# Kernel tuning notes

Hardware: AMD Instinct MI355X
Metric: run time of the kernel (lower is better)

The kernel has to match this reference:

```python
import jax, jax.numpy as jnp
import numpy as np

N = 8000      # nodes (spatial spots)
E = 40000     # directed edges (kNN graph, avg degree 5)
DIN = 1024    # input_dim
H = 3         # heads
C = 1024      # hidden_dim per head
NCLS = 460    # n_classes
NCEN = 100    # centroid count (pass-through only)
NEG_SLOPE = 0.2


def setup_inputs() -> dict:
    key = jax.random.key(0)
    ks = jax.random.split(key, 12)
    s_in = 1.0 / np.sqrt(DIN)   # glorot-ish scale for 1024 fan-in
    s_h = 1.0 / np.sqrt(C)
    return {
        'x': jax.random.normal(ks[0], (N, DIN), jnp.float32),
        'edge_index': jax.random.randint(ks[1], (E, 2), 0, N),  # [E,2] (src,dst)
        'Wl': jax.random.normal(ks[2], (DIN, H * C), jnp.float32) * s_in,
        'bl': jnp.zeros((H * C,), jnp.float32),
        'Wr': jax.random.normal(ks[3], (DIN, H * C), jnp.float32) * s_in,
        'br': jnp.zeros((H * C,), jnp.float32),
        'att': jax.random.normal(ks[4], (H, C), jnp.float32) * s_h,
        'bias': jnp.zeros((C,), jnp.float32),
        'Wf': jax.random.normal(ks[5], (C, NCLS), jnp.float32) * s_h,
        'bf': jnp.zeros((NCLS,), jnp.float32),
        'exps': jax.random.uniform(ks[6], (N, NCLS), jnp.float32),
        'exps_c': jax.random.uniform(ks[7], (NCEN, NCLS), jnp.float32),
    }


def reference(x, edge_index, Wl, bl, Wr, br, att, bias, Wf, bf, exps, exps_c):
    n = x.shape[0]
    h_, c_ = att.shape
    # PyG GATv2Conv default add_self_loops=True
    loops = jnp.arange(n)
    src = jnp.concatenate([edge_index[:, 0], loops])
    dst = jnp.concatenate([edge_index[:, 1], loops])
    # lin_l / lin_r projections -> [N,H,C]
    xl = (x @ Wl + bl).reshape(n, h_, c_)
    xr = (x @ Wr + br).reshape(n, h_, c_)
    # GATv2 edge scores: a^T LeakyReLU(x_l[src] + x_r[dst])  -> [Etot,H]
    s = jax.nn.leaky_relu(xl[src] + xr[dst], NEG_SLOPE)
    e = jnp.einsum('ehc,hc->eh', s, att)
    # segment softmax over incoming edges per dst node (PyG softmax: +1e-16)
    m = jax.lax.stop_gradient(jax.ops.segment_max(e, dst, num_segments=n))
    a = jnp.exp(e - m[dst])
    denom = jax.ops.segment_sum(a, dst, num_segments=n)
    alpha = a / (denom[dst] + 1e-16)
    # weighted scatter-add of source messages
    out = jax.ops.segment_sum(alpha[:, :, None] * xl[src], dst, num_segments=n)
    # concat=False -> mean over heads, then conv bias
    out = out.mean(axis=1) + bias
    # fc + row softmax
    h = jax.nn.softmax(out @ Wf + bf, axis=-1)
    return h
```

## Files before the change

### kernel.cpp

```cpp
#include <hip/hip_runtime.h>

#define NNODES 8000
#define MPAD   8192
#define NEDGES 40000
#define ETOT   (NEDGES + NNODES)
#define DIN    1024
#define NH     3
#define CH     1024
#define HC     (NH * CH)
#define NTOT   (2 * HC)
#define NCLS   460
#define NCLS_P 512
#define NEG    0.2f

typedef _Float16 h8 __attribute__((ext_vector_type(8)));
typedef _Float16 h4v __attribute__((ext_vector_type(4)));
typedef float    f4 __attribute__((ext_vector_type(4)));

#define GLOAD16(g, l) \
    __builtin_amdgcn_global_load_lds((const __attribute__((address_space(1))) void*)(g), \
                                     (__attribute__((address_space(3))) void*)(l), 16, 0, 0)

__global__ __launch_bounds__(256)
void fp16_pad_convert(const float* __restrict__ in, _Float16* __restrict__ out,
                      int rows_in, int rows_out, int cols)
{
    size_t i4 = (size_t)blockIdx.x * 256 + threadIdx.x;
    size_t tot = ((size_t)rows_out * cols) >> 2;
    if (i4 >= tot) return;
    size_t e = i4 << 2;
    int row = (int)(e / cols);
    float vx = 0.f, vy = 0.f, vz = 0.f, vw = 0.f;
    if (row < rows_in) {
        float4 v = *(const float4*)(in + e);
        vx = v.x; vy = v.y; vz = v.z; vw = v.w;
    }
    h4v o = { (_Float16)vx, (_Float16)vy, (_Float16)vz, (_Float16)vw };
    *(h4v*)(out + e) = o;
}

__global__ __launch_bounds__(256)
void transpose_to_fp16(const float* __restrict__ W, _Float16* __restrict__ Wt,
                       int K, int Ncols, int rowOff)
{
    __shared__ float tile[32][33];
    int n0 = blockIdx.x * 32, k0 = blockIdx.y * 32;
    int tx = threadIdx.x, ty = threadIdx.y;
    #pragma unroll
    for (int i = 0; i < 4; ++i) {
        int k = k0 + ty + i * 8;
        int n = n0 + tx;
        tile[ty + i * 8][tx] = (n < Ncols) ? W[(size_t)k * Ncols + n] : 0.f;
    }
    __syncthreads();
    #pragma unroll
    for (int i = 0; i < 4; ++i) {
        int n = n0 + ty + i * 8;
        int k = k0 + tx;
        Wt[(size_t)(rowOff + n) * K + k] = (_Float16)tile[tx][ty + i * 8];
    }
}

__global__ __launch_bounds__(256)
void bias_pack(const float* __restrict__ bl, const float* __restrict__ br,
               const float* __restrict__ bf, const float* __restrict__ att,
               float* __restrict__ b1, float* __restrict__ b2, _Float16* __restrict__ atth)
{
    int i = blockIdx.x * 256 + threadIdx.x;
    if (i < HC) { b1[i] = bl[i]; b1[HC + i] = br[i]; atth[i] = (_Float16)att[i]; }
    if (i < NCLS_P) b2[i] = (i < NCLS) ? bf[i] : 0.f;
}

__global__ __launch_bounds__(256)
void csr_count(const int* __restrict__ ei, int* __restrict__ cnt)
{
    int e = blockIdx.x * 256 + threadIdx.x;
    if (e >= ETOT) return;
    int dst = (e < NEDGES) ? ei[2 * e + 1] : (e - NEDGES);
    atomicAdd(&cnt[dst], 1);
}

__global__ __launch_bounds__(1024)
void csr_scan(const int* __restrict__ cnt, int* __restrict__ rofs)
{
    __shared__ int s[1024];
    int t = threadIdx.x;
    int base = t * 8;
    int local[8];
    int sum = 0;
    #pragma unroll
    for (int i = 0; i < 8; ++i) {
        local[i] = sum;
        sum += (base + i < NNODES) ? cnt[base + i] : 0;
    }
    s[t] = sum;
    __syncthreads();
    for (int off = 1; off < 1024; off <<= 1) {
        int v = (t >= off) ? s[t - off] : 0;
        __syncthreads();
        if (t >= off) s[t] += v;
        __syncthreads();
    }
    int pre = (t > 0) ? s[t - 1] : 0;
    #pragma unroll
    for (int i = 0; i < 8; ++i)
        if (base + i < NNODES) rofs[base + i] = pre + local[i];
}

__global__ __launch_bounds__(256)
void csr_fill(const int* __restrict__ ei, const int* __restrict__ rofs,
              int* __restrict__ cursor, int* __restrict__ csr_src)
{
    int e = blockIdx.x * 256 + threadIdx.x;
    if (e >= ETOT) return;
    int src, dst;
    if (e < NEDGES) { src = ei[2 * e]; dst = ei[2 * e + 1]; }
    else            { src = dst = e - NEDGES; }
    int pos = rofs[dst] + atomicAdd(&cursor[dst], 1);
    csr_src[pos] = src;
}

__global__ __launch_bounds__(512, 2)
void gemm256_f16(const _Float16* __restrict__ A, const _Float16* __restrict__ Bt,
                 const float* __restrict__ biasN, _Float16* __restrict__ C16,
                 int N, int K)
{
    __shared__ __align__(16) _Float16 lds[65536];

    int nwg = gridDim.x;
    int orig = blockIdx.x;
    int cpx = nwg >> 3;
    int wg = (orig & 7) * cpx + (orig >> 3);
    int nbx = N >> 8;
    int bm = wg / nbx, bn = wg - bm * nbx;
    int m0 = bm << 8, n0 = bn << 8;

    const int t = threadIdx.x;
    const int lane = t & 63;
    const int w = t >> 6;
    const int wm = w >> 2;
    const int wn = w & 3;

    const int sRow   = lane >> 3;
    const int sColSw = (((lane & 7) ^ sRow) << 3);
    const int seg0   = w << 1;

    const int l15 = lane & 15;

    f4 acc[8][4];
    f4 zero = { 0.f, 0.f, 0.f, 0.f };
    #pragma unroll
    for (int i = 0; i < 8; ++i)
        #pragma unroll
        for (int j = 0; j < 4; ++j) acc[i][j] = zero;

    auto STAGE_A = [&](int kt, int h, int b) {
        const _Float16* src = A + (size_t)(m0 + h * 128 + seg0 * 8 + sRow) * K + kt * 64 + sColSw;
        int dst = b * 32768 + h * 8192 + seg0 * 512;
        GLOAD16(src, &lds[dst]);
        GLOAD16(src + (size_t)8 * K, &lds[dst + 512]);
    };
    auto STAGE_B = [&](int kt, int h, int b) {
        const _Float16* src = Bt + (size_t)(n0 + h * 128 + seg0 * 8 + sRow) * K + kt * 64 + sColSw;
        int dst = b * 32768 + 16384 + h * 8192 + seg0 * 512;
        GLOAD16(src, &lds[dst]);
        GLOAD16(src + (size_t)8 * K, &lds[dst + 512]);
    };

    h8 bfr[4][2];
    const int aBase = wm * 128 + l15;
    const int bBase = wn * 64 + l15;

#define SWC(ks2) (((((ks2) * 4 + (lane >> 4)) ^ (l15 & 7)) << 3))
#define DS_A(fi, ks2, q, b) (*(const h8*)&lds[(b)*32768 + (aBase + (q)*32 + (fi)*16)*64 + SWC(ks2)])
#define DS_B(nf, ks2, b)    (*(const h8*)&lds[(b)*32768 + 16384 + (bBase + (nf)*16)*64 + SWC(ks2)])

#define PHASE(b, q, STAGE_STMT, VMEND)                                                            \
    {                                                                                             \
        h8 a00 = DS_A(0, 0, q, b), a01 = DS_A(0, 1, q, b);                                        \
        h8 a10 = DS_A(1, 0, q, b), a11 = DS_A(1, 1, q, b);                                        \
        if ((q) == 0) {                                                                           \
            _Pragma("unroll")                                                                     \
            for (int nf = 0; nf < 4; ++nf) {                                                      \
                bfr[nf][0] = DS_B(nf, 0, b);                                                      \
                bfr[nf][1] = DS_B(nf, 1, b);                                                      \
            }                                                                                     \
        }                                                                                         \
        STAGE_STMT;                                                                               \
        __builtin_amdgcn_s_barrier();                                                             \
        asm volatile("s_waitcnt lgkmcnt(0)" ::: "memory");                                        \
        __builtin_amdgcn_sched_barrier(0);                                                        \
        __builtin_amdgcn_s_setprio(1);                                                            \
        _Pragma("unroll")                                                                         \
        for (int nf = 0; nf < 4; ++nf) {                                                          \
            acc[(q)*2+0][nf] = __builtin_amdgcn_mfma_f32_16x16x32_f16(a00, bfr[nf][0], acc[(q)*2+0][nf], 0, 0, 0); \
            acc[(q)*2+0][nf] = __builtin_amdgcn_mfma_f32_16x16x32_f16(a01, bfr[nf][1], acc[(q)*2+0][nf], 0, 0, 0); \
            acc[(q)*2+1][nf] = __builtin_amdgcn_mfma_f32_16x16x32_f16(a10, bfr[nf][0], acc[(q)*2+1][nf], 0, 0, 0); \
            acc[(q)*2+1][nf] = __builtin_amdgcn_mfma_f32_16x16x32_f16(a11, bfr[nf][1], acc[(q)*2+1][nf], 0, 0, 0); \
        }                                                                                         \
        __builtin_amdgcn_s_setprio(0);                                                            \
        if (VMEND) asm volatile("s_waitcnt vmcnt(4)" ::: "memory");                               \
        __builtin_amdgcn_s_barrier();                                                             \
    }

    STAGE_A(0, 0, 0); STAGE_A(0, 1, 0);
    STAGE_B(0, 0, 0); STAGE_B(0, 1, 0);
    STAGE_B(1, 0, 1); STAGE_B(1, 1, 1);
    asm volatile("s_waitcnt vmcnt(4)" ::: "memory");
    __builtin_amdgcn_s_barrier();

    const int NKT = K >> 6;
    for (int kt = 0; kt < NKT; kt += 2) {
        PHASE(0, 0, STAGE_A(kt + 1, 0, 1), false);
        PHASE(0, 1, STAGE_A(kt + 1, 1, 1), false);
        PHASE(0, 2, STAGE_B(kt + 2, 0, 0), false);
        PHASE(0, 3, STAGE_B(kt + 2, 1, 0), true);
        PHASE(1, 0, STAGE_A(kt + 2, 0, 0), false);
        PHASE(1, 1, STAGE_A(kt + 2, 1, 0), false);
        PHASE(1, 2, STAGE_B(kt + 3, 0, 1), false);
        PHASE(1, 3, STAGE_B(kt + 3, 1, 1), true);
    }

#undef PHASE
#undef DS_A
#undef DS_B
#undef SWC

    #pragma unroll
    for (int mf = 0; mf < 8; ++mf) {
        int row0 = m0 + wm * 128 + mf * 16 + ((lane >> 4) << 2);
        #pragma unroll
        for (int nf = 0; nf < 4; ++nf) {
            int col = n0 + wn * 64 + nf * 16 + l15;
            float bb = biasN[col];
            #pragma unroll
            for (int rg = 0; rg < 4; ++rg)
                C16[(size_t)(row0 + rg) * N + col] = (_Float16)(acc[mf][nf][rg] + bb);
        }
    }
}

__global__ __launch_bounds__(256, 4)
void gemm_f16(const _Float16* __restrict__ A, const _Float16* __restrict__ Bt,
              const float* __restrict__ biasN,
              float* __restrict__ C32, _Float16* __restrict__ C16,
              int N, int K)
{
    __shared__ __align__(16) _Float16 sA[128 * 32];
    __shared__ __align__(16) _Float16 sB[128 * 32];

    int nwg = gridDim.x;
    int orig = blockIdx.x;
    int q = nwg >> 3, r = nwg & 7;
    int xcd = orig & 7, idx = orig >> 3;
    int wg = (xcd < r ? xcd * (q + 1) : r * (q + 1) + (xcd - r) * q) + idx;
    int nbx = N >> 7;
    int bm = wg / nbx, bn = wg - bm * nbx;
    int m0 = bm << 7, n0 = bn << 7;

    const int t = threadIdx.x;
    const int lane = t & 63, w = t >> 6;
    const int wr = (w >> 1) << 6, wc = (w & 1) << 6;

    f4 acc[4][4];
    f4 zero = { 0.f, 0.f, 0.f, 0.f };
    #pragma unroll
    for (int i = 0; i < 4; ++i)
        #pragma unroll
        for (int j = 0; j < 4; ++j) acc[i][j] = zero;

    const int lr = lane >> 2, lk = lane & 3;
    const _Float16* gA = A  + (size_t)(m0 + w * 16 + lr) * K + lk * 8;
    const _Float16* gB = Bt + (size_t)(n0 + w * 16 + lr) * K + lk * 8;
    _Float16* lA0 = &sA[w * 512];
    _Float16* lA1 = &sA[2048 + w * 512];
    _Float16* lB0 = &sB[w * 512];
    _Float16* lB1 = &sB[2048 + w * 512];
    const size_t seg = (size_t)64 * K;

    const int nk = K >> 5;
    for (int s = 0; s < nk; ++s) {
        const int ko = s << 5;
        GLOAD16(gA + ko,       lA0);
        GLOAD16(gA + seg + ko, lA1);
        GLOAD16(gB + ko,       lB0);
        GLOAD16(gB + seg + ko, lB1);
        __syncthreads();
        const int ks = lane >> 4;
        h8 bh[4];
        #pragma unroll
        for (int nj = 0; nj < 4; ++nj)
            bh[nj] = *(const h8*)&sB[(wc + nj * 16 + (lane & 15)) * 32 + ks * 8];
        #pragma unroll
        for (int mi = 0; mi < 4; ++mi) {
            h8 ah = *(const h8*)&sA[(wr + mi * 16 + (lane & 15)) * 32 + ks * 8];
            #pragma unroll
            for (int nj = 0; nj < 4; ++nj)
                acc[mi][nj] = __builtin_amdgcn_mfma_f32_16x16x32_f16(ah, bh[nj], acc[mi][nj], 0, 0, 0);
        }
        __syncthreads();
    }

    #pragma unroll
    for (int mi = 0; mi < 4; ++mi) {
        #pragma unroll
        for (int nj = 0; nj < 4; ++nj) {
            int col  = n0 + wc + nj * 16 + (lane & 15);
            int rowb = m0 + wr + mi * 16 + ((lane >> 4) << 2);
            float b = biasN[col];
            #pragma unroll
            for (int rg = 0; rg < 4; ++rg) {
                float v = acc[mi][nj][rg] + b;
                size_t off = (size_t)(rowb + rg) * N + col;
                if (C32) C32[off] = v;
                else     C16[off] = (_Float16)v;
            }
        }
    }
}

__global__ __launch_bounds__(192)
void edge_fused3(const _Float16* __restrict__ xlr, const int* __restrict__ rofs,
                 const int* __restrict__ cnt, const int* __restrict__ csr_src,
                 const _Float16* __restrict__ atth, const float* __restrict__ bias,
                 _Float16* __restrict__ o2h)
{
    __shared__ float comb[3 * CH];

    const int dst = blockIdx.x;
    const int h   = threadIdx.x >> 6;
    const int l   = threadIdx.x & 63;
    const int cb0 = l << 3, cb1 = 512 + (l << 3);

    const _Float16* pr = xlr + (size_t)dst * NTOT + HC + h * CH;
    h8 xr0 = *(const h8*)(pr + cb0);
    h8 xr1 = *(const h8*)(pr + cb1);
    h8 at0 = *(const h8*)(atth + h * CH + cb0);
    h8 at1 = *(const h8*)(atth + h * CH + cb1);

    const int beg = rofs[dst];
    const int num = cnt[dst];

    float m = -3.4e38f, d = 0.f;
    float a0[8] = {}, a1[8] = {};

    int src0 = csr_src[beg];
    const _Float16* p0 = xlr + (size_t)src0 * NTOT + h * CH;
    h8 nx0 = *(const h8*)(p0 + cb0);
    h8 nx1 = *(const h8*)(p0 + cb1);

    for (int i = 0; i < num; ++i) {
        h8 xv0 = nx0, xv1 = nx1;
        if (i + 1 < num) {
            int s2 = csr_src[beg + i + 1];
            const _Float16* p2 = xlr + (size_t)s2 * NTOT + h * CH;
            nx0 = *(const h8*)(p2 + cb0);
            nx1 = *(const h8*)(p2 + cb1);
        }
        float s = 0.f;
        #pragma unroll
        for (int j = 0; j < 8; ++j) {
            float z0 = (float)xv0[j] + (float)xr0[j];
            z0 = z0 > 0.f ? z0 : NEG * z0;
            s = fmaf((float)at0[j], z0, s);
            float z1 = (float)xv1[j] + (float)xr1[j];
            z1 = z1 > 0.f ? z1 : NEG * z1;
            s = fmaf((float)at1[j], z1, s);
        }
        #pragma unroll
        for (int off = 32; off > 0; off >>= 1) s += __shfl_xor(s, off);
        float nm = fmaxf(m, s);
        float rs = __expf(m - nm);
        float wt = __expf(s - nm);
        d = d * rs + wt;
        #pragma unroll
        for (int j = 0; j < 8; ++j) {
            a0[j] = fmaf(wt, (float)xv0[j], a0[j] * rs);
            a1[j] = fmaf(wt, (float)xv1[j], a1[j] * rs);
        }
        m = nm;
    }

    float inv = 1.f / (d + 1e-16f) * (1.f / 3.f);
    #pragma unroll
    for (int j = 0; j < 8; ++j) {
        comb[h * CH + cb0 + j] = a0[j] * inv;
        comb[h * CH + cb1 + j] = a1[j] * inv;
    }
    __syncthreads();

    if (threadIdx.x < 128) {
        int c = threadIdx.x << 3;
        h8 o;
        #pragma unroll
        for (int j = 0; j < 8; ++j) {
            float v = comb[c + j] + comb[CH + c + j] + comb[2 * CH + c + j] + bias[c + j];
            o[j] = (_Float16)v;
        }
        *(h8*)(o2h + (size_t)dst * CH + c) = o;
    }
}

__global__ __launch_bounds__(64)
void row_softmax(const float* __restrict__ logits, float* __restrict__ out)
{
    const int r = blockIdx.x;
    const int lane = threadIdx.x;
    const float* row = logits + (size_t)r * NCLS_P;
    float v[8];
    float mx = -3.4e38f;
    #pragma unroll
    for (int i = 0; i < 8; ++i) {
        int c = lane + i * 64;
        v[i] = (c < NCLS) ? row[c] : -3.4e38f;
        mx = fmaxf(mx, v[i]);
    }
    #pragma unroll
    for (int off = 32; off > 0; off >>= 1) mx = fmaxf(mx, __shfl_xor(mx, off));
    float s = 0.f;
    #pragma unroll
    for (int i = 0; i < 8; ++i) {
        int c = lane + i * 64;
        float ev = (c < NCLS) ? expf(v[i] - mx) : 0.f;
        v[i] = ev;
        s += ev;
    }
    #pragma unroll
    for (int off = 32; off > 0; off >>= 1) s += __shfl_xor(s, off);
    float inv = 1.f / s;
    #pragma unroll
    for (int i = 0; i < 8; ++i) {
        int c = lane + i * 64;
        if (c < NCLS) out[(size_t)r * NCLS + c] = v[i] * inv;
    }
}

extern "C" void kernel_launch(void* const* d_in, const int* in_sizes, int n_in,
                              void* d_out, int out_size, void* d_ws, size_t ws_size,
                              hipStream_t stream)
{
    (void)in_sizes; (void)n_in; (void)out_size; (void)ws_size;

    const float* x    = (const float*)d_in[0];
    const int*   ei   = (const int*)  d_in[1];
    const float* Wl   = (const float*)d_in[2];
    const float* bl   = (const float*)d_in[3];
    const float* Wr   = (const float*)d_in[4];
    const float* br   = (const float*)d_in[5];
    const float* att  = (const float*)d_in[6];
    const float* bias = (const float*)d_in[7];
    const float* Wf   = (const float*)d_in[8];
    const float* bf   = (const float*)d_in[9];

    char* base = (char*)d_ws;
    _Float16* xh      = (_Float16*)(base);
    _Float16* BtW     = (_Float16*)(base + 16777216);
    _Float16* Wft     = (_Float16*)(base + 29360128);
    float*    biasC1  = (float*)   (base + 30408704);
    float*    biasC2  = (float*)   (base + 30433280);
    _Float16* atth    = (_Float16*)(base + 30435328);
    int*      cnt     = (int*)     (base + 30441472);
    int*      cursor  = (int*)     (base + 30473472);
    int*      rofs    = (int*)     (base + 30505472);
    int*      csr_src = (int*)     (base + 30537472);
    _Float16* o2h     = (_Float16*)(base + 30729472);
    float*    logits  = (float*)   (base + 47506688);
    _Float16* xlr     = (_Float16*)(base + 64283904);

    hipMemsetAsync(cnt, 0, 64000, stream);
    hipMemsetAsync(o2h + (size_t)NNODES * CH, 0, (size_t)(MPAD - NNODES) * CH * 2, stream);

    fp16_pad_convert<<<(MPAD * DIN / 4 + 255) / 256, 256, 0, stream>>>(
        x, xh, NNODES, MPAD, DIN);

    transpose_to_fp16<<<dim3(HC / 32, DIN / 32), dim3(32, 8), 0, stream>>>(Wl, BtW, DIN, HC, 0);
    transpose_to_fp16<<<dim3(HC / 32, DIN / 32), dim3(32, 8), 0, stream>>>(Wr, BtW, DIN, HC, HC);
    transpose_to_fp16<<<dim3(NCLS_P / 32, DIN / 32), dim3(32, 8), 0, stream>>>(Wf, Wft, DIN, NCLS, 0);

    bias_pack<<<(HC + 255) / 256, 256, 0, stream>>>(bl, br, bf, att, biasC1, biasC2, atth);

    csr_count<<<(ETOT + 255) / 256, 256, 0, stream>>>(ei, cnt);
    csr_scan<<<1, 1024, 0, stream>>>(cnt, rofs);
    csr_fill<<<(ETOT + 255) / 256, 256, 0, stream>>>(ei, rofs, cursor, csr_src);

    gemm256_f16<<<(MPAD / 256) * (NTOT / 256), 512, 0, stream>>>(
        xh, BtW, biasC1, xlr, NTOT, DIN);

    edge_fused3<<<NNODES, 192, 0, stream>>>(xlr, rofs, cnt, csr_src, atth, bias, o2h);

    gemm_f16<<<(NCLS_P / 128) * (MPAD / 128), 256, 0, stream>>>(
        o2h, Wft, biasC2, logits, nullptr, NCLS_P, DIN);

    row_softmax<<<NNODES, 64, 0, stream>>>(logits, (float*)d_out);
}
```

Before: 351.3 us.

## Fuse fc GEMM with row softmax, merge prep kernels, double-prefetch edge gathers

Replaces the second GEMM plus a separate row_softmax with one kernel. Each block computes a 64-row by 512-column logit tile, stages it in shared memory and writes the softmax output directly, so the logits buffer never round-trips through global memory. It also merges the three transpose launches into one 3D grid and folds the CSR count into the bias-pack kernel, cutting launch count. It drops the o2h padding memset, which leaves the padded rows uninitialized; their results are never written out. The edge kernel now prefetches two edges ahead. The trade-off is a large shared-memory footprint and low per-block parallelism in the fused GEMM: 128 blocks, each loading all of Wf per k-step.

```diff
diff --git a/kernel.cpp b/kernel.cpp
--- a/kernel.cpp
+++ b/kernel.cpp
@@ -40,9 +40,19 @@
 }
 
 __global__ __launch_bounds__(256)
-void transpose_to_fp16(const float* __restrict__ W, _Float16* __restrict__ Wt,
-                       int K, int Ncols, int rowOff)
-{
+void transpose3(const float* __restrict__ Wl, const float* __restrict__ Wr,
+                const float* __restrict__ Wf, _Float16* __restrict__ BtW,
+                _Float16* __restrict__ Wft)
+{
+    const int z = blockIdx.z;
+    const float* W;
+    _Float16* out;
+    int Ncols, rowOff;
+    if (z == 0)      { W = Wl; out = BtW; Ncols = HC;   rowOff = 0;  }
+    else if (z == 1) { W = Wr; out = BtW; Ncols = HC;   rowOff = HC; }
+    else             { W = Wf; out = Wft; Ncols = NCLS; rowOff = 0;
+                       if (blockIdx.x >= NCLS_P / 32) return; }
+
     __shared__ float tile[32][33];
     int n0 = blockIdx.x * 32, k0 = blockIdx.y * 32;
     int tx = threadIdx.x, ty = threadIdx.y;
@@ -57,27 +67,24 @@
     for (int i = 0; i < 4; ++i) {
         int n = n0 + ty + i * 8;
         int k = k0 + tx;
-        Wt[(size_t)(rowOff + n) * K + k] = (_Float16)tile[tx][ty + i * 8];
+        out[(size_t)(rowOff + n) * DIN + k] = (_Float16)tile[tx][ty + i * 8];
     }
 }
 
 __global__ __launch_bounds__(256)
-void bias_pack(const float* __restrict__ bl, const float* __restrict__ br,
-               const float* __restrict__ bf, const float* __restrict__ att,
-               float* __restrict__ b1, float* __restrict__ b2, _Float16* __restrict__ atth)
+void prep_small(const float* __restrict__ bl, const float* __restrict__ br,
+                const float* __restrict__ bf, const float* __restrict__ att,
+                const int* __restrict__ ei,
+                float* __restrict__ b1, float* __restrict__ b2,
+                _Float16* __restrict__ atth, int* __restrict__ cnt)
 {
     int i = blockIdx.x * 256 + threadIdx.x;
     if (i < HC) { b1[i] = bl[i]; b1[HC + i] = br[i]; atth[i] = (_Float16)att[i]; }
     if (i < NCLS_P) b2[i] = (i < NCLS) ? bf[i] : 0.f;
-}
-
-__global__ __launch_bounds__(256)
-void csr_count(const int* __restrict__ ei, int* __restrict__ cnt)
-{
-    int e = blockIdx.x * 256 + threadIdx.x;
-    if (e >= ETOT) return;
-    int dst = (e < NEDGES) ? ei[2 * e + 1] : (e - NEDGES);
-    atomicAdd(&cnt[dst], 1);
+    if (i < ETOT) {
+        int dst = (i < NEDGES) ? ei[2 * i + 1] : (i - NEDGES);
+        atomicAdd(&cnt[dst], 1);
+    }
 }
 
 __global__ __launch_bounds__(1024)
@@ -240,82 +247,108 @@
     }
 }
 
-__global__ __launch_bounds__(256, 4)
-void gemm_f16(const _Float16* __restrict__ A, const _Float16* __restrict__ Bt,
-              const float* __restrict__ biasN,
-              float* __restrict__ C32, _Float16* __restrict__ C16,
-              int N, int K)
-{
-    __shared__ __align__(16) _Float16 sA[128 * 32];
-    __shared__ __align__(16) _Float16 sB[128 * 32];
-
-    int nwg = gridDim.x;
-    int orig = blockIdx.x;
-    int q = nwg >> 3, r = nwg & 7;
-    int xcd = orig & 7, idx = orig >> 3;
-    int wg = (xcd < r ? xcd * (q + 1) : r * (q + 1) + (xcd - r) * q) + idx;
-    int nbx = N >> 7;
-    int bm = wg / nbx, bn = wg - bm * nbx;
-    int m0 = bm << 7, n0 = bn << 7;
+__global__ __launch_bounds__(512, 2)
+void gemm2_sm(const _Float16* __restrict__ A, const _Float16* __restrict__ Bt,
+              const float* __restrict__ biasN, float* __restrict__ out)
+{
+    __shared__ __align__(16) char smem[66816];
+    _Float16* sAB  = (_Float16*)smem;
+    float*    sLog = (float*)smem;
+
+    const int bm = blockIdx.x;
+    const int m0 = bm << 6;
 
     const int t = threadIdx.x;
-    const int lane = t & 63, w = t >> 6;
-    const int wr = (w >> 1) << 6, wc = (w & 1) << 6;
-
-    f4 acc[4][4];
+    const int lane = t & 63;
+    const int w = t >> 6;
+    const int wm = w >> 2;
+    const int wn = w & 3;
+    const int l15 = lane & 15;
+    const int ks8 = (lane >> 4) << 3;
+
+    f4 acc[2][8];
     f4 zero = { 0.f, 0.f, 0.f, 0.f };
     #pragma unroll
-    for (int i = 0; i < 4; ++i)
-        #pragma unroll
-        for (int j = 0; j < 4; ++j) acc[i][j] = zero;
-
-    const int lr = lane >> 2, lk = lane & 3;
-    const _Float16* gA = A  + (size_t)(m0 + w * 16 + lr) * K + lk * 8;
-    const _Float16* gB = Bt + (size_t)(n0 + w * 16 + lr) * K + lk * 8;
-    _Float16* lA0 = &sA[w * 512];
-    _Float16* lA1 = &sA[2048 + w * 512];
-    _Float16* lB0 = &sB[w * 512];
-    _Float16* lB1 = &sB[2048 + w * 512];
-    const size_t seg = (size_t)64 * K;
-
-    const int nk = K >> 5;
-    for (int s = 0; s < nk; ++s) {
+    for (int i = 0; i < 2; ++i)
+        #pragma unroll
+        for (int j = 0; j < 8; ++j) acc[i][j] = zero;
+
+    const int sr = lane >> 2, sc = (lane & 3) << 3;
+    const _Float16* gA = A  + (size_t)(m0 + w * 16 + sr) * DIN + sc;
+    const _Float16* gB = Bt + (size_t)(w * 64 + sr) * DIN + sc;
+
+    for (int s = 0; s < DIN / 32; ++s) {
         const int ko = s << 5;
-        GLOAD16(gA + ko,       lA0);
-        GLOAD16(gA + seg + ko, lA1);
-        GLOAD16(gB + ko,       lB0);
-        GLOAD16(gB + seg + ko, lB1);
-        __syncthreads();
-        const int ks = lane >> 4;
-        h8 bh[4];
-        #pragma unroll
-        for (int nj = 0; nj < 4; ++nj)
-            bh[nj] = *(const h8*)&sB[(wc + nj * 16 + (lane & 15)) * 32 + ks * 8];
-        #pragma unroll
-        for (int mi = 0; mi < 4; ++mi) {
-            h8 ah = *(const h8*)&sA[(wr + mi * 16 + (lane & 15)) * 32 + ks * 8];
-            #pragma unroll
-            for (int nj = 0; nj < 4; ++nj)
-                acc[mi][nj] = __builtin_amdgcn_mfma_f32_16x16x32_f16(ah, bh[nj], acc[mi][nj], 0, 0, 0);
-        }
-        __syncthreads();
-    }
-
-    #pragma unroll
-    for (int mi = 0; mi < 4; ++mi) {
-        #pragma unroll
-        for (int nj = 0; nj < 4; ++nj) {
-            int col  = n0 + wc + nj * 16 + (lane & 15);
-            int rowb = m0 + wr + mi * 16 + ((lane >> 4) << 2);
-            float b = biasN[col];
-            #pragma unroll
-            for (int rg = 0; rg < 4; ++rg) {
-                float v = acc[mi][nj][rg] + b;
-                size_t off = (size_t)(rowb + rg) * N + col;
-                if (C32) C32[off] = v;
-                else     C16[off] = (_Float16)v;
+        if (w < 4) GLOAD16(gA + ko, &sAB[w * 512]);
+        #pragma unroll
+        for (int j = 0; j < 4; ++j)
+            GLOAD16(gB + (size_t)j * 16 * DIN + ko, &sAB[2048 + (w * 4 + j) * 512]);
+        __syncthreads();
+        h8 bh[8];
+        #pragma unroll
+        for (int nf = 0; nf < 8; ++nf)
+            bh[nf] = *(const h8*)&sAB[2048 + (wn * 128 + nf * 16 + l15) * 32 + ks8];
+        #pragma unroll
+        for (int mi = 0; mi < 2; ++mi) {
+            h8 ah = *(const h8*)&sAB[(wm * 32 + mi * 16 + l15) * 32 + ks8];
+            #pragma unroll
+            for (int nf = 0; nf < 8; ++nf)
+                acc[mi][nf] = __builtin_amdgcn_mfma_f32_16x16x32_f16(ah, bh[nf], acc[mi][nf], 0, 0, 0);
+        }
+        __syncthreads();
+    }
+
+    for (int hh = 0; hh < 2; ++hh) {
+        if (wm == hh) {
+            #pragma unroll
+            for (int mi = 0; mi < 2; ++mi) {
+                int lrow = mi * 16 + ((lane >> 4) << 2);
+                #pragma unroll
+                for (int nf = 0; nf < 8; ++nf) {
+                    int col = wn * 128 + nf * 16 + l15;
+                    float b = biasN[col];
+                    #pragma unroll
+                    for (int rg = 0; rg < 4; ++rg)
+                        sLog[(lrow + rg) * 521 + col] = acc[mi][nf][rg] + b;
+                }
             }
         }
+        __syncthreads();
+        {
+            int lrow = t >> 4;
+            int s16  = t & 15;
+            int grow = m0 + hh * 32 + lrow;
+            float vbuf[32];
+            float mx = -3.4e38f;
+            #pragma unroll
+            for (int k = 0; k < 32; ++k) {
+                int col = s16 + (k << 4);
+                float v = (col < NCLS) ? sLog[lrow * 521 + col] : -3.4e38f;
+                vbuf[k] = v;
+                mx = fmaxf(mx, v);
+            }
+            #pragma unroll
+            for (int off = 8; off > 0; off >>= 1) mx = fmaxf(mx, __shfl_xor(mx, off));
+            float sum = 0.f;
+            #pragma unroll
+            for (int k = 0; k < 32; ++k) {
+                int col = s16 + (k << 4);
+                float e = (col < NCLS) ? __expf(vbuf[k] - mx) : 0.f;
+                vbuf[k] = e;
+                sum += e;
+            }
+            #pragma unroll
+            for (int off = 8; off > 0; off >>= 1) sum += __shfl_xor(sum, off);
+            float inv = 1.f / sum;
+            if (grow < NNODES) {
+                #pragma unroll
+                for (int k = 0; k < 32; ++k) {
+                    int col = s16 + (k << 4);
+                    if (col < NCLS) out[(size_t)grow * NCLS + col] = vbuf[k] * inv;
+                }
+            }
+        }
+        __syncthreads();
     }
 }
 
@@ -344,18 +377,28 @@
     float m = -3.4e38f, d = 0.f;
     float a0[8] = {}, a1[8] = {};
 
-    int src0 = csr_src[beg];
-    const _Float16* p0 = xlr + (size_t)src0 * NTOT + h * CH;
-    h8 nx0 = *(const h8*)(p0 + cb0);
-    h8 nx1 = *(const h8*)(p0 + cb1);
-
+    int srcA = csr_src[beg];
+    const _Float16* pA = xlr + (size_t)srcA * NTOT + h * CH;
+    h8 eA0 = *(const h8*)(pA + cb0), eA1 = *(const h8*)(pA + cb1);
+    h8 eB0 = eA0, eB1 = eA1;
+    if (num > 1) {
+        int srcB = csr_src[beg + 1];
+        const _Float16* pB = xlr + (size_t)srcB * NTOT + h * CH;
+        eB0 = *(const h8*)(pB + cb0);
+        eB1 = *(const h8*)(pB + cb1);
+    }
+
+    #pragma unroll 2
     for (int i = 0; i < num; ++i) {
-        h8 xv0 = nx0, xv1 = nx1;
-        if (i + 1 < num) {
-            int s2 = csr_src[beg + i + 1];
+        const bool odd = (i & 1) != 0;
+        h8 xv0 = odd ? eB0 : eA0;
+        h8 xv1 = odd ? eB1 : eA1;
+        if (i + 2 < num) {
+            int s2 = csr_src[beg + i + 2];
             const _Float16* p2 = xlr + (size_t)s2 * NTOT + h * CH;
-            nx0 = *(const h8*)(p2 + cb0);
-            nx1 = *(const h8*)(p2 + cb1);
+            h8 n0 = *(const h8*)(p2 + cb0);
+            h8 n1 = *(const h8*)(p2 + cb1);
+            if (odd) { eB0 = n0; eB1 = n1; } else { eA0 = n0; eA1 = n1; }
         }
         float s = 0.f;
         #pragma unroll
@@ -398,40 +441,6 @@
             o[j] = (_Float16)v;
         }
         *(h8*)(o2h + (size_t)dst * CH + c) = o;
-    }
-}
-
-__global__ __launch_bounds__(64)
-void row_softmax(const float* __restrict__ logits, float* __restrict__ out)
-{
-    const int r = blockIdx.x;
-    const int lane = threadIdx.x;
-    const float* row = logits + (size_t)r * NCLS_P;
-    float v[8];
-    float mx = -3.4e38f;
-    #pragma unroll
-    for (int i = 0; i < 8; ++i) {
-        int c = lane + i * 64;
-        v[i] = (c < NCLS) ? row[c] : -3.4e38f;
-        mx = fmaxf(mx, v[i]);
-    }
-    #pragma unroll
-    for (int off = 32; off > 0; off >>= 1) mx = fmaxf(mx, __shfl_xor(mx, off));
-    float s = 0.f;
-    #pragma unroll
-    for (int i = 0; i < 8; ++i) {
-        int c = lane + i * 64;
-        float ev = (c < NCLS) ? expf(v[i] - mx) : 0.f;
-        v[i] = ev;
-        s += ev;
-    }
-    #pragma unroll
-    for (int off = 32; off > 0; off >>= 1) s += __shfl_xor(s, off);
-    float inv = 1.f / s;
-    #pragma unroll
-    for (int i = 0; i < 8; ++i) {
-        int c = lane + i * 64;
-        if (c < NCLS) out[(size_t)r * NCLS + c] = v[i] * inv;
     }
 }
 
@@ -464,22 +473,19 @@
     int*      rofs    = (int*)     (base + 30505472);
     int*      csr_src = (int*)     (base + 30537472);
     _Float16* o2h     = (_Float16*)(base + 30729472);
-    float*    logits  = (float*)   (base + 47506688);
     _Float16* xlr     = (_Float16*)(base + 64283904);
 
     hipMemsetAsync(cnt, 0, 64000, stream);
-    hipMemsetAsync(o2h + (size_t)NNODES * CH, 0, (size_t)(MPAD - NNODES) * CH * 2, stream);
 
     fp16_pad_convert<<<(MPAD * DIN / 4 + 255) / 256, 256, 0, stream>>>(
         x, xh, NNODES, MPAD, DIN);
 
-    transpose_to_fp16<<<dim3(HC / 32, DIN / 32), dim3(32, 8), 0, stream>>>(Wl, BtW, DIN, HC, 0);
-    transpose_to_fp16<<<dim3(HC / 32, DIN / 32), dim3(32, 8), 0, stream>>>(Wr, BtW, DIN, HC, HC);
-    transpose_to_fp16<<<dim3(NCLS_P / 32, DIN / 32), dim3(32, 8), 0, stream>>>(Wf, Wft, DIN, NCLS, 0);
-
-    bias_pack<<<(HC + 255) / 256, 256, 0, stream>>>(bl, br, bf, att, biasC1, biasC2, atth);
-
-    csr_count<<<(ETOT + 255) / 256, 256, 0, stream>>>(ei, cnt);
+    transpose3<<<dim3(HC / 32, DIN / 32, 3), dim3(32, 8), 0, stream>>>(
+        Wl, Wr, Wf, BtW, Wft);
+
+    prep_small<<<(ETOT + 255) / 256, 256, 0, stream>>>(
+        bl, br, bf, att, ei, biasC1, biasC2, atth, cnt);
+
     csr_scan<<<1, 1024, 0, stream>>>(cnt, rofs);
     csr_fill<<<(ETOT + 255) / 256, 256, 0, stream>>>(ei, rofs, cursor, csr_src);
 
@@ -488,8 +494,5 @@
 
     edge_fused3<<<NNODES, 192, 0, stream>>>(xlr, rofs, cnt, csr_src, atth, bias, o2h);
 
-    gemm_f16<<<(NCLS_P / 128) * (MPAD / 128), 256, 0, stream>>>(
-        o2h, Wft, biasC2, logits, nullptr, NCLS_P, DIN);
-
-    row_softmax<<<NNODES, 64, 0, stream>>>(logits, (float*)d_out);
-}
+    gemm2_sm<<<MPAD / 64, 512, 0, stream>>>(o2h, Wft, biasC2, (float*)d_out);
+}
```

New measurement: 354.3 us. No clear change (+0.9%).
